# Kernel optimization log

Hardware: AMD Instinct MI355X
Metric: run time of the kernel (lower is better)

Reference implementation:

```python
import jax, jax.numpy as jnp
import numpy as np

B, C, H, W = 32, 384, 32, 32
NH = 4            # num_heads
CC = 192          # conv_channels = ceil(384/2)
HID = 1536        # mlp hidden = 4*dim
EPS = 1e-6


def _ln2d(x, w, b):
    # LayerNorm over channel axis of NCHW
    u = x.mean(1, keepdims=True)
    s = ((x - u) ** 2).mean(1, keepdims=True)
    return w[:, None, None] * ((x - u) * jax.lax.rsqrt(s + EPS)) + b[:, None, None]


def setup_inputs() -> dict:
    key = jax.random.key(0)
    ks = jax.random.split(key, 8)
    f = lambda k, shp, sc: jax.random.normal(k, shp, jnp.float32) * sc
    return {
        "x": f(ks[0], (B, C, H, W), 1.0),
        "conv_w": f(ks[1], (CC, 1, 3, 3), 0.1),
        "conv_b": jnp.zeros((CC,), jnp.float32),
        "nxca_w": jnp.ones((C,), jnp.float32),
        "nxca_b": jnp.zeros((C,), jnp.float32),
        "temp": jnp.ones((NH, 1, 1), jnp.float32),
        "qkv_w": f(ks[2], (3 * C, C), 0.05),
        "qkv_b": jnp.zeros((3 * C,), jnp.float32),
        "proj_w": f(ks[3], (C, C), 0.05),
        "proj_b": jnp.zeros((C,), jnp.float32),
        "norm_w": jnp.ones((C,), jnp.float32),
        "norm_b": jnp.zeros((C,), jnp.float32),
        "fc1_w": f(ks[4], (HID, C), 0.05),
        "fc1_b": jnp.zeros((HID,), jnp.float32),
        "fc2_w": f(ks[5], (C, HID), 0.05),
        "fc2_b": jnp.zeros((C,), jnp.float32),
        "gamma_xca": jnp.ones((C,), jnp.float32),
        "gamma": jnp.ones((C,), jnp.float32),
    }


def reference(x, conv_w, conv_b, nxca_w, nxca_b, temp, qkv_w, qkv_b,
              proj_w, proj_b, norm_w, norm_b, fc1_w, fc1_b, fc2_w, fc2_b,
              gamma_xca, gamma):
    b, c, h, w = x.shape
    n = h * w
    hd = c // NH
    # depthwise 3x3 conv on first CC channels (in-place in torch -> shortcut
    # taken AFTER the conv, faithfully reproduced here)
    xc = jax.lax.conv_general_dilated(
        x[:, :CC], conv_w, (1, 1), ((1, 1), (1, 1)), feature_group_count=CC
    ) + conv_b[None, :, None, None]
    x = jnp.concatenate([xc, x[:, CC:]], axis=1)
    shortcut = x
    # XCA branch
    y = _ln2d(x, nxca_w, nxca_b)
    yf = y.reshape(b, c, n).transpose(0, 2, 1)                       # [B,N,C]
    qkv = (yf @ qkv_w.T + qkv_b).reshape(b, n, 3, NH, hd).transpose(2, 0, 3, 1, 4)
    q, k, v = qkv[0], qkv[1], qkv[2]                                  # [B,h,N,hd]
    q = q / jnp.maximum(jnp.linalg.norm(q, axis=-1, keepdims=True), 1e-12)
    k = k / jnp.maximum(jnp.linalg.norm(k, axis=-1, keepdims=True), 1e-12)
    attn = jax.nn.softmax(jnp.einsum('bhnd,bhmd->bhnm', q, k) * temp, axis=-1)
    o = jnp.einsum('bhnm,bhmd->bhnd', attn, v).transpose(0, 2, 1, 3).reshape(b, n, c)
    o = (o @ proj_w.T + proj_b).transpose(0, 2, 1).reshape(b, c, h, w)
    x = shortcut + gamma_xca[None, :, None, None] * o
    # MLP branch
    shortcut2 = x
    z = _ln2d(x, norm_w, norm_b).transpose(0, 2, 3, 1).reshape(b, n, c)
    z = jax.nn.gelu(z @ fc1_w.T + fc1_b, approximate=False) @ fc2_w.T + fc2_b
    z = z.reshape(b, h, w, c).transpose(0, 3, 1, 2)
    return shortcut2 + gamma[None, :, None, None] * z
```

## Files before the change

kernel.cpp:

```cpp
#include <hip/hip_runtime.h>
#include <cstdint>

typedef unsigned short u16;
typedef unsigned int u32;
typedef unsigned long long u64;
typedef __attribute__((ext_vector_type(4))) float f32x4;
typedef __attribute__((ext_vector_type(8))) __bf16 bf16x8;
typedef __attribute__((ext_vector_type(8))) u16 u16x8;

#define DEV __device__ __forceinline__

DEV u16 cvt16(float f) {
  __bf16 h = (__bf16)f;
  return __builtin_bit_cast(u16, h);
}
DEV u16 f2bf(float f) {
  u32 u = __builtin_bit_cast(u32, f);
  u += 0x7fffu + ((u >> 16) & 1u);
  return (u16)(u >> 16);
}
DEV float bflo2f(u32 packed) { return __builtin_bit_cast(float, packed << 16); }
DEV float bfhi2f(u32 packed) { return __builtin_bit_cast(float, packed & 0xffff0000u); }

DEV void g2l16(void* lds_wave_base, const void* gsrc) {
  __builtin_amdgcn_global_load_lds(
      (const __attribute__((address_space(1))) u32*)gsrc,
      (__attribute__((address_space(3))) u32*)lds_wave_base, 16, 0, 0);
}

DEV float gelu_tanh(float v) {
  float z = v * (0.7978845608f + 0.0356774081f * v * v);
  float e = __expf(2.0f * z);
  float th = 1.0f - 2.0f / (e + 1.0f);
  return 0.5f * v * (1.0f + th);
}

__global__ __launch_bounds__(256) void conv_k(const float* __restrict__ x,
                                              const float* __restrict__ cw,
                                              const float* __restrict__ cb,
                                              float* __restrict__ xc) {
  const int bc = blockIdx.x;
  const int c = bc % 384;
  const int p4 = threadIdx.x * 4;
  const float* xp = x + ((size_t)bc << 10);
  float* op = xc + ((size_t)bc << 10) + p4;
  if (c >= 192) {
    *(f32x4*)op = *(const f32x4*)(xp + p4);
    return;
  }
  const int hh = p4 >> 5, ww0 = p4 & 31;
  const float* wb = cw + c * 9;
  float b0 = cb[c];
  float a0 = b0, a1 = b0, a2 = b0, a3 = b0;
#pragma unroll
  for (int dy = 0; dy < 3; ++dy) {
    int y = hh + dy - 1;
    if ((unsigned)y < 32u) {
      const float* rp = xp + y * 32 + ww0;
      f32x4 m = *(const f32x4*)rp;
      float lft = (ww0 > 0) ? rp[-1] : 0.f;
      float rgt = (ww0 < 28) ? rp[4] : 0.f;
      float w0 = wb[dy * 3], w1 = wb[dy * 3 + 1], w2 = wb[dy * 3 + 2];
      a0 += lft * w0 + m[0] * w1 + m[1] * w2;
      a1 += m[0] * w0 + m[1] * w1 + m[2] * w2;
      a2 += m[1] * w0 + m[2] * w1 + m[3] * w2;
      a3 += m[2] * w0 + m[3] * w1 + rgt * w2;
    }
  }
  f32x4 r = {a0, a1, a2, a3};
  *(f32x4*)op = r;
}

__global__ __launch_bounds__(256) void cvt4_k(const float* __restrict__ s0,
                                              const float* __restrict__ s1,
                                              const float* __restrict__ s2,
                                              const float* __restrict__ s3,
                                              u16* __restrict__ d0,
                                              u16* __restrict__ d1,
                                              u16* __restrict__ d2,
                                              u16* __restrict__ d3) {
  int id = blockIdx.x * 256 + threadIdx.x;
  if (id < 442368) d0[id] = f2bf(s0[id]);
  else if (id < 589824) d1[id - 442368] = f2bf(s1[id - 442368]);
  else if (id < 1179648) d2[id - 589824] = f2bf(s2[id - 589824]);
  else if (id < 1769472) d3[id - 1179648] = f2bf(s3[id - 1179648]);
}

__global__ __launch_bounds__(256) void ln_t_k(const float* __restrict__ X,
                                              const float* __restrict__ w,
                                              const float* __restrict__ bsh,
                                              u16* __restrict__ Y) {
  __shared__ float tile[384][33];
  __shared__ float ps[8][32], ps2[8][32];
  __shared__ float mean_s[32], rstd_s[32];
  const int b = blockIdx.y;
  const int p0 = blockIdx.x * 32;
  const int t = threadIdx.x;
  const int pl = t & 31, cg = t >> 5;
  const float* xb = X + (((size_t)b * 384) << 10) + p0 + pl;
  float s = 0.f, s2 = 0.f;
  for (int c = cg; c < 384; c += 8) {
    float v = xb[(size_t)c << 10];
    tile[c][pl] = v;
    s += v;
    s2 += v * v;
  }
  ps[cg][pl] = s;
  ps2[cg][pl] = s2;
  __syncthreads();
  if (t < 32) {
    float a = 0.f, a2 = 0.f;
#pragma unroll
    for (int g = 0; g < 8; ++g) { a += ps[g][t]; a2 += ps2[g][t]; }
    float mu = a * (1.f / 384.f);
    float var = a2 * (1.f / 384.f) - mu * mu;
    mean_s[t] = mu;
    rstd_s[t] = rsqrtf(var + 1e-6f);
  }
  __syncthreads();
  const int cl = t & 63, pg = t >> 6;
  for (int p = pg; p < 32; p += 4) {
    float mu = mean_s[p], rs = rstd_s[p];
    size_t orow = (((size_t)b << 10) + p0 + p) * 384;
#pragma unroll
    for (int cc = 0; cc < 6; ++cc) {
      int c = cc * 64 + cl;
      float v = (tile[c][p] - mu) * rs * w[c] + bsh[c];
      Y[orow + c] = f2bf(v);
    }
  }
}

__global__ __launch_bounds__(256) void normk_k(u16* __restrict__ QKV) {
  const int t = threadIdx.x;
  const int w = t >> 6, l = t & 63;
  const int rg = l >> 4, li = l & 15;
  const int tok = blockIdx.x * 16 + w * 4 + rg;
  u16* rowp = QKV + (size_t)tok * 1152 + 384;
#pragma unroll
  for (int h = 0; h < 4; ++h) {
    u16* p = rowp + h * 96 + li * 6;
    u32 a = *(const u32*)p;
    u32 b2 = *(const u32*)(p + 2);
    u32 c = *(const u32*)(p + 4);
    float v[6] = {bflo2f(a), bfhi2f(a), bflo2f(b2), bfhi2f(b2), bflo2f(c), bfhi2f(c)};
    float ss = 0.f;
#pragma unroll
    for (int i = 0; i < 6; ++i) ss += v[i] * v[i];
#pragma unroll
    for (int mk = 1; mk < 16; mk <<= 1) ss += __shfl_xor(ss, mk, 64);
    float sc = 1.0f / fmaxf(sqrtf(ss), 1e-12f);
    u32 o0 = (u32)f2bf(v[0] * sc) | ((u32)f2bf(v[1] * sc) << 16);
    u32 o1 = (u32)f2bf(v[2] * sc) | ((u32)f2bf(v[3] * sc) << 16);
    u32 o2 = (u32)f2bf(v[4] * sc) | ((u32)f2bf(v[5] * sc) << 16);
    *(u32*)p = o0;
    *(u32*)(p + 2) = o1;
    *(u32*)(p + 4) = o2;
  }
}

__global__ __launch_bounds__(256) void attn_k(const u16* __restrict__ QKV,
                                              const u16* __restrict__ Vg,
                                              u16* __restrict__ O,
                                              const float* __restrict__ temp) {
  __shared__ u16 Kt[2][8192];
  __shared__ u16 Vt[2][6144];
  __shared__ u16 Pt[4][2304];
  const int t = threadIdx.x;
  const int w = t >> 6, l = t & 63;
  const int l15 = l & 15, kg = l >> 4;
  const int id = blockIdx.x;
  const int xcd = id & 7, jj = id >> 3;
  const int bh = xcd * 16 + (jj >> 3);
  const int qb = jj & 7;
  const int b = bh >> 2, h = bh & 3;
  const int q0 = qb * 128 + w * 32;
  const u16* Qb = QKV + (size_t)b * 1024 * 1152;
  const char* Kbg = (const char*)QKV + (size_t)b * 1024 * 2304 + 768 + 192 * h;
  const u16* Vbg = Vg + (size_t)bh * 98304;
  const float tl2e = temp[h] * 1.44269504f;
  const float mT2 = -fabsf(temp[h]) * 1.44269504f;

  u32 sK[4], sV[3];
#pragma unroll
  for (int j = 0; j < 4; ++j) {
    u32 s = w * 4096 + j * 1024 + l * 16;
    u32 row = s >> 8, rem = s & 255;
    u32 X = rem ^ ((row & 7) << 4);
    sK[j] = (X < 192) ? (row * 2304 + X) : 0u;
  }
#pragma unroll
  for (int j = 0; j < 3; ++j) {
    u32 s = w * 3072 + j * 1024 + l * 16;
    u32 u = s ^ (((s >> 7) & 7) << 4);
    sV[j] = (u >> 7) * 2048 + (u & 127);
  }
  u32 cs[3];
#pragma unroll
  for (int kk = 0; kk < 3; ++kk)
    cs[kk] = (u32)((kk * 64 + kg * 16) ^ ((l15 & 7) << 4));

  bf16x8 qf[2][3];
#pragma unroll
  for (int f = 0; f < 2; ++f) {
    const u16* qp = Qb + (size_t)(q0 + f * 16 + l15) * 1152 + h * 96 + kg * 8;
#pragma unroll
    for (int kk = 0; kk < 3; ++kk) qf[f][kk] = *(const bf16x8*)(qp + kk * 32);
  }
  float a0[4], a1[4];
  {
    float alpha[2];
#pragma unroll
    for (int f = 0; f < 2; ++f) {
      float ss = 0.f;
#pragma unroll
      for (int kk = 0; kk < 3; ++kk)
#pragma unroll
        for (int e = 0; e < 8; ++e) {
          float v = (float)qf[f][kk][e];
          ss += v * v;
        }
      ss += __shfl_xor(ss, 16, 64);
      ss += __shfl_xor(ss, 32, 64);
      alpha[f] = tl2e * rsqrtf(fmaxf(ss, 1e-24f));
    }
#pragma unroll
    for (int j = 0; j < 4; ++j) {
      a0[j] = __shfl(alpha[0], kg * 4 + j, 64);
      a1[j] = __shfl(alpha[1], kg * 4 + j, 64);
    }
  }
  f32x4 oa[2][6];
#pragma unroll
  for (int f = 0; f < 2; ++f)
#pragma unroll
    for (int d = 0; d < 6; ++d) oa[f][d] = {0.f, 0.f, 0.f, 0.f};
  float l_r[2][4] = {{0.f, 0.f, 0.f, 0.f}, {0.f, 0.f, 0.f, 0.f}};
  __bf16* Pw = (__bf16*)&Pt[w][0];

#define STAGE(buf, kv0)                                                        \
  {                                                                            \
    const char* kb = Kbg + (size_t)(kv0) * 2304;                               \
    const char* vb = (const char*)Vbg + (size_t)(kv0) * 2;                     \
    char* kd = (char*)&Kt[buf][0] + w * 4096;                                  \
    char* vd = (char*)&Vt[buf][0] + w * 3072;                                  \
    g2l16(kd, kb + sK[0]);                                                     \
    g2l16(kd + 1024, kb + sK[1]);                                              \
    g2l16(kd + 2048, kb + sK[2]);                                              \
    g2l16(kd + 3072, kb + sK[3]);                                              \
    g2l16(vd, vb + sV[0]);                                                     \
    g2l16(vd + 1024, vb + sV[1]);                                              \
    g2l16(vd + 2048, vb + sV[2]);                                              \
  }

  STAGE(0, 0);
  for (int tt = 0; tt < 16; ++tt) {
    const int cur = tt & 1;
    if (tt < 15) {
      STAGE(cur ^ 1, (tt + 1) * 64);
      asm volatile("s_waitcnt vmcnt(7)" ::: "memory");
    } else {
      asm volatile("s_waitcnt vmcnt(0)" ::: "memory");
    }
    __builtin_amdgcn_s_barrier();
    const char* Kc = (const char*)&Kt[cur][0];
    const char* Vc = (const char*)&Vt[cur][0];
    f32x4 s0[4], s1[4];
#pragma unroll
    for (int n = 0; n < 4; ++n) { s0[n] = {0.f, 0.f, 0.f, 0.f}; s1[n] = {0.f, 0.f, 0.f, 0.f}; }
    __builtin_amdgcn_s_setprio(1);
#pragma unroll
    for (int n = 0; n < 4; ++n) {
      const char* krow = Kc + ((n * 16 + l15) << 8);
#pragma unroll
      for (int kk = 0; kk < 3; ++kk) {
        bf16x8 kf = *(const bf16x8*)(krow + cs[kk]);
        s0[n] = __builtin_amdgcn_mfma_f32_16x16x32_bf16(qf[0][kk], kf, s0[n], 0, 0, 0);
        s1[n] = __builtin_amdgcn_mfma_f32_16x16x32_bf16(qf[1][kk], kf, s1[n], 0, 0, 0);
      }
    }
    __builtin_amdgcn_s_setprio(0);
#pragma unroll
    for (int n = 0; n < 4; ++n) {
#pragma unroll
      for (int j = 0; j < 4; ++j) {
        float p0 = exp2f(fmaf(s0[n][j], a0[j], mT2));
        float p1 = exp2f(fmaf(s1[n][j], a1[j], mT2));
        l_r[0][j] += p0;
        l_r[1][j] += p1;
        Pw[(kg * 4 + j) * 72 + n * 16 + l15] = (__bf16)p0;
        Pw[(16 + kg * 4 + j) * 72 + n * 16 + l15] = (__bf16)p1;
      }
    }
    __builtin_amdgcn_s_setprio(1);
#pragma unroll
    for (int kk = 0; kk < 2; ++kk) {
      bf16x8 pf0 = *(const bf16x8*)(Pw + (size_t)l15 * 72 + kk * 32 + kg * 8);
      bf16x8 pf1 = *(const bf16x8*)(Pw + (size_t)(16 + l15) * 72 + kk * 32 + kg * 8);
#pragma unroll
      for (int d = 0; d < 6; ++d) {
        bf16x8 vf = *(const bf16x8*)(Vc + ((d * 16 + l15) << 7) + cs[kk]);
        oa[0][d] = __builtin_amdgcn_mfma_f32_16x16x32_bf16(pf0, vf, oa[0][d], 0, 0, 0);
        oa[1][d] = __builtin_amdgcn_mfma_f32_16x16x32_bf16(pf1, vf, oa[1][d], 0, 0, 0);
      }
    }
    __builtin_amdgcn_s_setprio(0);
    __builtin_amdgcn_s_barrier();
  }
#undef STAGE
  float inv[2][4];
#pragma unroll
  for (int f = 0; f < 2; ++f)
#pragma unroll
    for (int j = 0; j < 4; ++j) {
      float sum = l_r[f][j];
#pragma unroll
      for (int mk = 1; mk < 16; mk <<= 1) sum += __shfl_xor(sum, mk, 64);
      inv[f][j] = 1.0f / sum;
    }
#pragma unroll
  for (int f = 0; f < 2; ++f)
#pragma unroll
    for (int d = 0; d < 6; ++d)
#pragma unroll
      for (int j = 0; j < 4; ++j) {
        int tok = q0 + f * 16 + kg * 4 + j;
        O[((size_t)b * 1024 + tok) * 384 + h * 96 + d * 16 + l15] =
            f2bf(oa[f][d][j] * inv[f][j]);
      }
}

template <int EPI>
__global__ __launch_bounds__(512) void gemm256_k(const u16* __restrict__ A,
                                                 const u16* __restrict__ B,
                                                 int N, int K,
                                                 const float* __restrict__ bias,
                                                 u16* __restrict__ vtp,
                                                 u16* __restrict__ outp,
                                                 int nbx) {
  __shared__ u16 SM[24576];
  const int t = threadIdx.x;
  const int w = t >> 6, l = t & 63;
  const int l15 = l & 15, kg = l >> 4;
  const int id = blockIdx.x;
  const int xcd = id & 7, jj = id >> 3;
  const int qq = jj / nbx;
  const int bx = jj - qq * nbx;
  const int by = xcd * 16 + qq;
  const int m0 = by * 256, n0 = bx * 128;
  const int wr = w >> 1, wc = w & 1;
  const size_t ldab = (size_t)K * 2;
  const char* pa1 = (const char*)A + (size_t)(m0 + (t >> 2)) * ldab + (t & 3) * 16;
  const char* pa2 = pa1 + (size_t)128 * ldab;
  const char* pb1 = (const char*)B + (size_t)(n0 + (t >> 2)) * ldab + (t & 3) * 16;
  char* SMc = (char*)SM;

  f32x4 acc[4][4];
#pragma unroll
  for (int m = 0; m < 4; ++m)
#pragma unroll
    for (int n = 0; n < 4; ++n) acc[m][n] = {0.f, 0.f, 0.f, 0.f};

  const int nkt = K >> 5;
  g2l16(SMc + w * 1024, pa1);
  g2l16(SMc + 8192 + w * 1024, pa2);
  g2l16(SMc + 32768 + w * 1024, pb1);
  for (int kt = 0; kt < nkt; ++kt) {
    const int buf = kt & 1;
    if (kt + 1 < nkt) {
      const size_t o = (size_t)(kt + 1) * 64;
      g2l16(SMc + (buf ^ 1) * 16384 + w * 1024, pa1 + o);
      g2l16(SMc + (buf ^ 1) * 16384 + 8192 + w * 1024, pa2 + o);
      g2l16(SMc + 32768 + (buf ^ 1) * 8192 + w * 1024, pb1 + o);
      asm volatile("s_waitcnt vmcnt(3)" ::: "memory");
    } else {
      asm volatile("s_waitcnt vmcnt(0)" ::: "memory");
    }
    __builtin_amdgcn_s_barrier();
    __builtin_amdgcn_sched_barrier(0);
    const u16* Ab = SM + buf * 8192;
    const u16* Bb = SM + 16384 + buf * 4096;
    bf16x8 af[4], bfr[4];
#pragma unroll
    for (int m = 0; m < 4; ++m)
      af[m] = *(const bf16x8*)(Ab + (wr * 64 + m * 16 + l15) * 32 + kg * 8);
#pragma unroll
    for (int n = 0; n < 4; ++n)
      bfr[n] = *(const bf16x8*)(Bb + (wc * 64 + n * 16 + l15) * 32 + kg * 8);
    __builtin_amdgcn_s_setprio(1);
#pragma unroll
    for (int m = 0; m < 4; ++m)
#pragma unroll
      for (int n = 0; n < 4; ++n)
        acc[m][n] = __builtin_amdgcn_mfma_f32_16x16x32_bf16(af[m], bfr[n], acc[m][n], 0, 0, 0);
    __builtin_amdgcn_s_setprio(0);
    __builtin_amdgcn_sched_barrier(0);
    __builtin_amdgcn_s_barrier();
  }

  if (EPI == 4 && n0 >= 768) {
#pragma unroll
    for (int m = 0; m < 4; ++m) {
      const int tokbase = m0 + wr * 64 + m * 16 + kg * 4;
      const int bb = tokbase >> 10, nb = tokbase & 1023;
#pragma unroll
      for (int n = 0; n < 4; ++n) {
        int within = n0 - 768 + wc * 64 + n * 16 + l15;
        int hh = within / 96;
        int dd = within - hh * 96;
        float bs = bias[768 + within];
        int bh = bb * 4 + hh;
        u64 pk = 0;
#pragma unroll
        for (int j = 0; j < 4; ++j)
          pk |= (u64)cvt16(acc[m][n][j] + bs) << (16 * j);
        *(u64*)(vtp + ((size_t)bh * 96 + dd) * 1024 + nb) = pk;
      }
    }
    return;
  }

  u16* Ct = SM;
  float bs[4];
#pragma unroll
  for (int n = 0; n < 4; ++n) bs[n] = bias[n0 + wc * 64 + n * 16 + l15];
  const size_t ostride = (EPI == 4) ? 1152 : (size_t)N;
#pragma unroll
  for (int p = 0; p < 2; ++p) {
    if ((wr >> 1) == p) {
      u16* cw_ = Ct + ((wr & 1) * 64 + kg * 4) * 128 + wc * 64 + l15;
#pragma unroll
      for (int m = 0; m < 4; ++m)
#pragma unroll
        for (int n = 0; n < 4; ++n)
#pragma unroll
          for (int j = 0; j < 4; ++j) {
            float v = acc[m][n][j] + bs[n];
            if (EPI == 1) v = gelu_tanh(v);
            cw_[(m * 16 + j) * 128 + n * 16] = cvt16(v);
          }
    }
    __syncthreads();
    const int row_l = t >> 2;
    const int colc = (t & 3) * 32;
    const u16* src = Ct + row_l * 128 + colc;
    u16* dst = outp + (size_t)(m0 + p * 128 + row_l) * ostride + n0 + colc;
#pragma unroll
    for (int c4 = 0; c4 < 4; ++c4)
      *(u16x8*)(dst + c4 * 8) = *(const u16x8*)(src + c4 * 8);
    __syncthreads();
  }
}

__global__ __launch_bounds__(256) void gemm_k(const u16* __restrict__ A,
                                              const u16* __restrict__ B,
                                              int K,
                                              const float* __restrict__ bias,
                                              const float* __restrict__ gamma,
                                              const float* __restrict__ res,
                                              float* __restrict__ outp) {
  __shared__ u16 SM[16384];
  const int t = threadIdx.x;
  const int w = t >> 6, l = t & 63;
  const int l15 = l & 15, kg = l >> 4;
  int id = blockIdx.x;
  int xcd = id & 7, jj = id >> 3;
  int by = jj % 3;
  int bx = (jj / 3) * 8 + xcd;
  const int m0 = by * 128, n0 = bx * 128;
  const int wr = w >> 1, wc = w & 1;

  const size_t ldab = (size_t)K * 2;
  const char* pa1 = (const char*)A + (size_t)(m0 + (t >> 2)) * ldab + (t & 3) * 16;
  const char* pa2 = pa1 + (size_t)64 * ldab;
  const char* pb1 = (const char*)B + (size_t)(n0 + (t >> 2)) * ldab + (t & 3) * 16;
  const char* pb2 = pb1 + (size_t)64 * ldab;
  char* SMc = (char*)SM;

  f32x4 acc[4][4];
#pragma unroll
  for (int m = 0; m < 4; ++m)
#pragma unroll
    for (int n = 0; n < 4; ++n) acc[m][n] = {0.f, 0.f, 0.f, 0.f};

  const int nkt = K >> 5;
  {
    char* ad = SMc + w * 1024;
    char* bd = SMc + 16384 + w * 1024;
    g2l16(ad, pa1); g2l16(ad + 4096, pa2);
    g2l16(bd, pb1); g2l16(bd + 4096, pb2);
  }
  for (int kt = 0; kt < nkt; ++kt) {
    const int buf = kt & 1;
    if (kt + 1 < nkt) {
      const size_t o = (size_t)(kt + 1) * 64;
      char* ad = SMc + (buf ^ 1) * 8192 + w * 1024;
      char* bd = SMc + 16384 + (buf ^ 1) * 8192 + w * 1024;
      g2l16(ad, pa1 + o); g2l16(ad + 4096, pa2 + o);
      g2l16(bd, pb1 + o); g2l16(bd + 4096, pb2 + o);
      asm volatile("s_waitcnt vmcnt(4)" ::: "memory");
    } else {
      asm volatile("s_waitcnt vmcnt(0)" ::: "memory");
    }
    __builtin_amdgcn_s_barrier();
    __builtin_amdgcn_sched_barrier(0);
    const u16* Ab = SM + buf * 4096;
    const u16* Bb = SM + 8192 + buf * 4096;
    bf16x8 af[4], bfr[4];
#pragma unroll
    for (int m = 0; m < 4; ++m)
      af[m] = *(const bf16x8*)(Ab + (wr * 64 + m * 16 + l15) * 32 + kg * 8);
#pragma unroll
    for (int n = 0; n < 4; ++n)
      bfr[n] = *(const bf16x8*)(Bb + (wc * 64 + n * 16 + l15) * 32 + kg * 8);
    __builtin_amdgcn_s_setprio(1);
#pragma unroll
    for (int m = 0; m < 4; ++m)
#pragma unroll
      for (int n = 0; n < 4; ++n)
        acc[m][n] = __builtin_amdgcn_mfma_f32_16x16x32_bf16(af[m], bfr[n], acc[m][n], 0, 0, 0);
    __builtin_amdgcn_s_setprio(0);
    __builtin_amdgcn_sched_barrier(0);
    __builtin_amdgcn_s_barrier();
  }

#pragma unroll
  for (int m = 0; m < 4; ++m) {
#pragma unroll
    for (int n = 0; n < 4; ++n) {
      int tok = n0 + wc * 64 + n * 16 + l15;
      int bb = tok >> 10, p = tok & 1023;
#pragma unroll
      for (int j = 0; j < 4; ++j) {
        int c = m0 + wr * 64 + m * 16 + kg * 4 + j;
        size_t addr = (((size_t)(bb * 384 + c)) << 10) + p;
        outp[addr] = res[addr] + gamma[c] * (acc[m][n][j] + bias[c]);
      }
    }
  }
}

extern "C" void kernel_launch(void* const* d_in, const int* in_sizes, int n_in,
                              void* d_out, int out_size, void* d_ws,
                              size_t ws_size, hipStream_t stream) {
  const float* x      = (const float*)d_in[0];
  const float* conv_w = (const float*)d_in[1];
  const float* conv_b = (const float*)d_in[2];
  const float* nxca_w = (const float*)d_in[3];
  const float* nxca_b = (const float*)d_in[4];
  const float* temp   = (const float*)d_in[5];
  const float* qkv_w  = (const float*)d_in[6];
  const float* qkv_b  = (const float*)d_in[7];
  const float* proj_w = (const float*)d_in[8];
  const float* proj_b = (const float*)d_in[9];
  const float* norm_w = (const float*)d_in[10];
  const float* norm_b = (const float*)d_in[11];
  const float* fc1_w  = (const float*)d_in[12];
  const float* fc1_b  = (const float*)d_in[13];
  const float* fc2_w  = (const float*)d_in[14];
  const float* fc2_b  = (const float*)d_in[15];
  const float* g_xca  = (const float*)d_in[16];
  const float* g_mlp  = (const float*)d_in[17];
  (void)in_sizes; (void)n_in; (void)out_size; (void)ws_size;

  char* ws = (char*)d_ws;
  float* xc  = (float*)(ws);
  u16* Y     = (u16*)(ws + 50331648);
  u16* QKVr  = (u16*)(ws + 75497472);
  u16* Vt    = (u16*)(ws + 150994944);
  u16* Obuf  = Y;
  u16* H1    = QKVr;
  u16* wq    = (u16*)(ws + 176160768);
  u16* wp    = (u16*)(ws + 177045504);
  u16* w1    = (u16*)(ws + 177340416);
  u16* w2    = (u16*)(ws + 178520064);

  cvt4_k<<<6912, 256, 0, stream>>>(qkv_w, proj_w, fc1_w, fc2_w, wq, wp, w1, w2);

  conv_k<<<12288, 256, 0, stream>>>(x, conv_w, conv_b, xc);
  ln_t_k<<<dim3(32, 32), 256, 0, stream>>>(xc, nxca_w, nxca_b, Y);
  gemm256_k<4><<<1152, 512, 0, stream>>>(Y, wq, 1152, 384, qkv_b, Vt, QKVr, 9);
  normk_k<<<2048, 256, 0, stream>>>(QKVr);
  attn_k<<<1024, 256, 0, stream>>>(QKVr, Vt, Obuf, temp);
  gemm_k<<<768, 256, 0, stream>>>(wp, Obuf, 384, proj_b, g_xca, xc, xc);
  ln_t_k<<<dim3(32, 32), 256, 0, stream>>>(xc, norm_w, norm_b, Y);
  gemm256_k<1><<<1536, 512, 0, stream>>>(Y, w1, 1536, 384, fc1_b, nullptr, H1, 12);
  gemm_k<<<768, 256, 0, stream>>>(w2, H1, 1536, fc2_b, g_mlp, xc, (float*)d_out);
}
```

Measured before the change: 411.6 us.

## Rewrite attention with 32x32 MFMA, transposed scores and register-resident P

Rebuilds the attention kernel around 32x32x16 bf16 MFMA, computing S transposed (K as the A operand) so that each lane holds one query's column of scores. The probabilities are then rearranged into PV operand layout with permlane32_swap instead of a round trip through an LDS scratch buffer. The K tile is packed unpadded at 208-byte rows to shrink LDS, and the kernel declares an occupancy hint of 3 blocks. The aim is to remove the P LDS writes, reads and row shuffles and to raise occupancy. The risks are register pressure under the new launch bound and LDS bank conflicts from the unswizzled K stride.

```diff
diff --git a/kernel.cpp b/kernel.cpp
--- a/kernel.cpp
+++ b/kernel.cpp
@@ -5,8 +5,11 @@
 typedef unsigned int u32;
 typedef unsigned long long u64;
 typedef __attribute__((ext_vector_type(4))) float f32x4;
+typedef __attribute__((ext_vector_type(16))) float f32x16;
 typedef __attribute__((ext_vector_type(8))) __bf16 bf16x8;
 typedef __attribute__((ext_vector_type(8))) u16 u16x8;
+typedef __attribute__((ext_vector_type(4))) u32 u32x4;
+typedef __attribute__((ext_vector_type(2))) int i32x2;
 
 #define DEV __device__ __forceinline__
 
@@ -159,16 +162,15 @@
   }
 }
 
-__global__ __launch_bounds__(256) void attn_k(const u16* __restrict__ QKV,
-                                              const u16* __restrict__ Vg,
-                                              u16* __restrict__ O,
-                                              const float* __restrict__ temp) {
-  __shared__ u16 Kt[2][8192];
+__global__ __launch_bounds__(256, 3) void attn_k(const u16* __restrict__ QKV,
+                                                 const u16* __restrict__ Vg,
+                                                 u16* __restrict__ O,
+                                                 const float* __restrict__ temp) {
+  __shared__ u16 Kt[2][6656];
   __shared__ u16 Vt[2][6144];
-  __shared__ u16 Pt[4][2304];
   const int t = threadIdx.x;
   const int w = t >> 6, l = t & 63;
-  const int l15 = l & 15, kg = l >> 4;
+  const int l31 = l & 31, hi = l >> 5;
   const int id = blockIdx.x;
   const int xcd = id & 7, jj = id >> 3;
   const int bh = xcd * 16 + (jj >> 3);
@@ -177,80 +179,64 @@
   const int q0 = qb * 128 + w * 32;
   const u16* Qb = QKV + (size_t)b * 1024 * 1152;
   const char* Kbg = (const char*)QKV + (size_t)b * 1024 * 2304 + 768 + 192 * h;
-  const u16* Vbg = Vg + (size_t)bh * 98304;
+  const char* Vbg = (const char*)(Vg + (size_t)bh * 98304);
   const float tl2e = temp[h] * 1.44269504f;
   const float mT2 = -fabsf(temp[h]) * 1.44269504f;
 
-  u32 sK[4], sV[3];
-#pragma unroll
-  for (int j = 0; j < 4; ++j) {
-    u32 s = w * 4096 + j * 1024 + l * 16;
-    u32 row = s >> 8, rem = s & 255;
-    u32 X = rem ^ ((row & 7) << 4);
-    sK[j] = (X < 192) ? (row * 2304 + X) : 0u;
-  }
-#pragma unroll
-  for (int j = 0; j < 3; ++j) {
-    u32 s = w * 3072 + j * 1024 + l * 16;
-    u32 u = s ^ (((s >> 7) & 7) << 4);
-    sV[j] = (u >> 7) * 2048 + (u & 127);
-  }
-  u32 cs[3];
-#pragma unroll
-  for (int kk = 0; kk < 3; ++kk)
-    cs[kk] = (u32)((kk * 64 + kg * 16) ^ ((l15 & 7) << 4));
-
-  bf16x8 qf[2][3];
-#pragma unroll
-  for (int f = 0; f < 2; ++f) {
-    const u16* qp = Qb + (size_t)(q0 + f * 16 + l15) * 1152 + h * 96 + kg * 8;
-#pragma unroll
-    for (int kk = 0; kk < 3; ++kk) qf[f][kk] = *(const bf16x8*)(qp + kk * 32);
-  }
-  float a0[4], a1[4];
+  u32 kOff[4], vOff[3];
+#pragma unroll
+  for (int i = 0; i < 4; ++i) {
+    int s = (i < 3) ? (i * 256 + t) : (768 + w * 16 + (l & 15));
+    int row = s / 13, c = s - row * 13;
+    kOff[i] = row * 2304 + ((c < 12) ? c * 16 : 0);
+  }
+#pragma unroll
+  for (int i = 0; i < 3; ++i) {
+    int s = i * 256 + t;
+    int row = s >> 3, cb = (s & 7) * 16;
+    vOff[i] = row * 2048 + (cb ^ ((row & 7) << 4));
+  }
+
+  bf16x8 qf[6];
   {
-    float alpha[2];
-#pragma unroll
-    for (int f = 0; f < 2; ++f) {
-      float ss = 0.f;
-#pragma unroll
-      for (int kk = 0; kk < 3; ++kk)
-#pragma unroll
-        for (int e = 0; e < 8; ++e) {
-          float v = (float)qf[f][kk][e];
-          ss += v * v;
-        }
-      ss += __shfl_xor(ss, 16, 64);
-      ss += __shfl_xor(ss, 32, 64);
-      alpha[f] = tl2e * rsqrtf(fmaxf(ss, 1e-24f));
-    }
-#pragma unroll
-    for (int j = 0; j < 4; ++j) {
-      a0[j] = __shfl(alpha[0], kg * 4 + j, 64);
-      a1[j] = __shfl(alpha[1], kg * 4 + j, 64);
-    }
-  }
-  f32x4 oa[2][6];
-#pragma unroll
-  for (int f = 0; f < 2; ++f)
-#pragma unroll
-    for (int d = 0; d < 6; ++d) oa[f][d] = {0.f, 0.f, 0.f, 0.f};
-  float l_r[2][4] = {{0.f, 0.f, 0.f, 0.f}, {0.f, 0.f, 0.f, 0.f}};
-  __bf16* Pw = (__bf16*)&Pt[w][0];
+    const u16* qp = Qb + (size_t)(q0 + l31) * 1152 + h * 96 + hi * 8;
+#pragma unroll
+    for (int kc = 0; kc < 6; ++kc) qf[kc] = *(const bf16x8*)(qp + kc * 16);
+  }
+  float alpha;
+  {
+    float ss = 0.f;
+#pragma unroll
+    for (int kc = 0; kc < 6; ++kc)
+#pragma unroll
+      for (int e = 0; e < 8; ++e) {
+        float v = (float)qf[kc][e];
+        ss += v * v;
+      }
+    ss += __shfl_xor(ss, 32, 64);
+    alpha = tl2e * rsqrtf(fmaxf(ss, 1e-24f));
+  }
+
+  f32x16 oa[3];
+#pragma unroll
+  for (int dt = 0; dt < 3; ++dt)
+#pragma unroll
+    for (int r = 0; r < 16; ++r) oa[dt][r] = 0.f;
+  float l_r = 0.f;
 
 #define STAGE(buf, kv0)                                                        \
   {                                                                            \
     const char* kb = Kbg + (size_t)(kv0) * 2304;                               \
-    const char* vb = (const char*)Vbg + (size_t)(kv0) * 2;                     \
-    char* kd = (char*)&Kt[buf][0] + w * 4096;                                  \
-    char* vd = (char*)&Vt[buf][0] + w * 3072;                                  \
-    g2l16(kd, kb + sK[0]);                                                     \
-    g2l16(kd + 1024, kb + sK[1]);                                              \
-    g2l16(kd + 2048, kb + sK[2]);                                              \
-    g2l16(kd + 3072, kb + sK[3]);                                              \
-    g2l16(vd, vb + sV[0]);                                                     \
-    g2l16(vd + 1024, vb + sV[1]);                                              \
-    g2l16(vd + 2048, vb + sV[2]);                                              \
+    const char* vb = Vbg + (size_t)(kv0) * 2;                                  \
+    char* kd = (char*)&Kt[buf][0];                                             \
+    char* vd = (char*)&Vt[buf][0];                                             \
+    g2l16(kd + w * 1024, kb + kOff[0]);                                        \
+    g2l16(kd + 4096 + w * 1024, kb + kOff[1]);                                 \
+    g2l16(kd + 8192 + w * 1024, kb + kOff[2]);                                 \
+    if (l < 16) g2l16(kd + 12288 + w * 256, kb + kOff[3]);                     \
+    g2l16(vd + w * 1024, vb + vOff[0]);                                        \
+    g2l16(vd + 4096 + w * 1024, vb + vOff[1]);                                 \
+    g2l16(vd + 8192 + w * 1024, vb + vOff[2]);                                 \
   }
 
   STAGE(0, 0);
@@ -265,69 +251,66 @@
     __builtin_amdgcn_s_barrier();
     const char* Kc = (const char*)&Kt[cur][0];
     const char* Vc = (const char*)&Vt[cur][0];
-    f32x4 s0[4], s1[4];
-#pragma unroll
-    for (int n = 0; n < 4; ++n) { s0[n] = {0.f, 0.f, 0.f, 0.f}; s1[n] = {0.f, 0.f, 0.f, 0.f}; }
-    __builtin_amdgcn_s_setprio(1);
-#pragma unroll
-    for (int n = 0; n < 4; ++n) {
-      const char* krow = Kc + ((n * 16 + l15) << 8);
-#pragma unroll
-      for (int kk = 0; kk < 3; ++kk) {
-        bf16x8 kf = *(const bf16x8*)(krow + cs[kk]);
-        s0[n] = __builtin_amdgcn_mfma_f32_16x16x32_bf16(qf[0][kk], kf, s0[n], 0, 0, 0);
-        s1[n] = __builtin_amdgcn_mfma_f32_16x16x32_bf16(qf[1][kk], kf, s1[n], 0, 0, 0);
+    f32x16 st[2];
+#pragma unroll
+    for (int n = 0; n < 2; ++n)
+#pragma unroll
+      for (int r = 0; r < 16; ++r) st[n][r] = 0.f;
+#pragma unroll
+    for (int n = 0; n < 2; ++n) {
+      const char* krow = Kc + (n * 32 + l31) * 208 + hi * 16;
+#pragma unroll
+      for (int kc = 0; kc < 6; ++kc) {
+        bf16x8 kf = *(const bf16x8*)(krow + kc * 32);
+        st[n] = __builtin_amdgcn_mfma_f32_32x32x16_bf16(kf, qf[kc], st[n], 0, 0, 0);
       }
     }
-    __builtin_amdgcn_s_setprio(0);
-#pragma unroll
-    for (int n = 0; n < 4; ++n) {
-#pragma unroll
-      for (int j = 0; j < 4; ++j) {
-        float p0 = exp2f(fmaf(s0[n][j], a0[j], mT2));
-        float p1 = exp2f(fmaf(s1[n][j], a1[j], mT2));
-        l_r[0][j] += p0;
-        l_r[1][j] += p1;
-        Pw[(kg * 4 + j) * 72 + n * 16 + l15] = (__bf16)p0;
-        Pw[(16 + kg * 4 + j) * 72 + n * 16 + l15] = (__bf16)p1;
+    u32 pk[2][8];
+#pragma unroll
+    for (int n = 0; n < 2; ++n) {
+      float p[16];
+#pragma unroll
+      for (int r = 0; r < 16; ++r) {
+        p[r] = exp2f(fmaf(st[n][r], alpha, mT2));
+        l_r += p[r];
       }
-    }
-    __builtin_amdgcn_s_setprio(1);
-#pragma unroll
-    for (int kk = 0; kk < 2; ++kk) {
-      bf16x8 pf0 = *(const bf16x8*)(Pw + (size_t)l15 * 72 + kk * 32 + kg * 8);
-      bf16x8 pf1 = *(const bf16x8*)(Pw + (size_t)(16 + l15) * 72 + kk * 32 + kg * 8);
-#pragma unroll
-      for (int d = 0; d < 6; ++d) {
-        bf16x8 vf = *(const bf16x8*)(Vc + ((d * 16 + l15) << 7) + cs[kk]);
-        oa[0][d] = __builtin_amdgcn_mfma_f32_16x16x32_bf16(pf0, vf, oa[0][d], 0, 0, 0);
-        oa[1][d] = __builtin_amdgcn_mfma_f32_16x16x32_bf16(pf1, vf, oa[1][d], 0, 0, 0);
+#pragma unroll
+      for (int m = 0; m < 8; ++m)
+        pk[n][m] = (u32)cvt16(p[2 * m]) | ((u32)cvt16(p[2 * m + 1]) << 16);
+    }
+#pragma unroll
+    for (int c = 0; c < 4; ++c) {
+      const int n = c >> 1, cc = c & 1;
+      i32x2 s1 = __builtin_amdgcn_permlane32_swap((int)pk[n][4 * cc],
+                                                  (int)pk[n][4 * cc + 2], 0, 0);
+      i32x2 s2 = __builtin_amdgcn_permlane32_swap((int)pk[n][4 * cc + 1],
+                                                  (int)pk[n][4 * cc + 3], 0, 0);
+      u32x4 wd;
+      wd[0] = (u32)s1[0]; wd[1] = (u32)s2[0];
+      wd[2] = (u32)s1[1]; wd[3] = (u32)s2[1];
+      bf16x8 pa = __builtin_bit_cast(bf16x8, wd);
+      const u32 vcol = (u32)((c * 32 + hi * 16) ^ ((l31 & 7) << 4));
+#pragma unroll
+      for (int dt = 0; dt < 3; ++dt) {
+        bf16x8 vf = *(const bf16x8*)(Vc + (dt * 32 + l31) * 128 + vcol);
+        oa[dt] = __builtin_amdgcn_mfma_f32_32x32x16_bf16(pa, vf, oa[dt], 0, 0, 0);
       }
     }
-    __builtin_amdgcn_s_setprio(0);
     __builtin_amdgcn_s_barrier();
   }
 #undef STAGE
-  float inv[2][4];
-#pragma unroll
-  for (int f = 0; f < 2; ++f)
-#pragma unroll
-    for (int j = 0; j < 4; ++j) {
-      float sum = l_r[f][j];
-#pragma unroll
-      for (int mk = 1; mk < 16; mk <<= 1) sum += __shfl_xor(sum, mk, 64);
-      inv[f][j] = 1.0f / sum;
-    }
-#pragma unroll
-  for (int f = 0; f < 2; ++f)
-#pragma unroll
-    for (int d = 0; d < 6; ++d)
-#pragma unroll
-      for (int j = 0; j < 4; ++j) {
-        int tok = q0 + f * 16 + kg * 4 + j;
-        O[((size_t)b * 1024 + tok) * 384 + h * 96 + d * 16 + l15] =
-            f2bf(oa[f][d][j] * inv[f][j]);
-      }
+  l_r += __shfl_xor(l_r, 32, 64);
+  float inv = 1.0f / l_r;
+#pragma unroll
+  for (int r = 0; r < 16; ++r) {
+    const int qr = (r & 3) + 8 * (r >> 2) + 4 * hi;
+    float invr = __shfl(inv, qr, 64);
+    const int tok = q0 + qr;
+    u16* orow = O + ((size_t)b * 1024 + tok) * 384 + h * 96;
+#pragma unroll
+    for (int dt = 0; dt < 3; ++dt)
+      orow[dt * 32 + l31] = f2bf(oa[dt][r] * invr);
+  }
 }
 
 template <int EPI>
```

New measurement: 396.1 us. -3.8%, faster.
